# Kernel optimization log

Hardware: AMD Instinct MI355X
Metric: run time of the kernel (lower is better)

## Reference

```python
import jax, jax.numpy as jnp
import numpy as np

H = 2048       # hidden_size
NH = 16        # num_attention_heads
NKV = 4        # num_key_value_heads
HD = H // NH   # head_dim = 128
INTER = 8192   # intermediate_size
L = 2048       # packed sequence length
EPS = 1e-6


def rmsnorm(x, w, eps=EPS):
    var = jnp.mean(x * x, axis=-1, keepdims=True)
    return x * jax.lax.rsqrt(var + eps) * w


def setup_inputs() -> dict:
    key = jax.random.key(0)
    ks = jax.random.split(key, 9)
    s = 0.02
    return {
        "hidden_states": jax.random.normal(ks[0], (1, L, H), jnp.float32),
        "cu_seqlens_q": jnp.array([0, 512, 1280, 2048], jnp.int32),
        "ln1_w": jnp.ones((H,), jnp.float32),
        "ln2_w": jnp.ones((H,), jnp.float32),
        "q_w": jax.random.normal(ks[1], (NH * HD, H), jnp.float32) * s,
        "k_w": jax.random.normal(ks[2], (NKV * HD, H), jnp.float32) * s,
        "v_w": jax.random.normal(ks[3], (NKV * HD, H), jnp.float32) * s,
        "o_w": jax.random.normal(ks[4], (H, NH * HD), jnp.float32) * s,
        "gate_w": jax.random.normal(ks[5], (INTER, H), jnp.float32) * s,
        "up_w": jax.random.normal(ks[6], (INTER, H), jnp.float32) * s,
        "down_w": jax.random.normal(ks[7], (H, INTER), jnp.float32) * s,
    }


def _segment_mask(cu, q_len):
    # segment id of each position: repeat_interleave of arange over lengths
    pos = jnp.arange(q_len)
    seg = jnp.searchsorted(cu[1:], pos, side="right")  # [L]
    mask = seg[:, None] == seg[None, :]
    mask = mask & (pos[None, :] <= pos[:, None])  # causal, q_len == k_len
    return mask  # [L, L] bool


def _forward(hidden_states, cu_seqlens_q, ln1_w, ln2_w, q_w, k_w, v_w, o_w,
             gate_w, up_w, down_w):
    b, q_len, _ = hidden_states.shape
    residual = hidden_states
    normed = rmsnorm(hidden_states, ln1_w)

    # project_kv
    key_states = (normed @ k_w.T).reshape(b, q_len, NKV, HD)
    value_states = (normed @ v_w.T).reshape(b, q_len, NKV, HD)

    q = (normed @ q_w.T).reshape(b, q_len, NH, HD)
    rep = NH // NKV
    k = jnp.repeat(key_states, rep, axis=2)   # repeat_interleave over heads
    v = jnp.repeat(value_states, rep, axis=2)

    scores = jnp.einsum("bqhd,bkhd->bhqk", q, k) / np.sqrt(HD)
    mask = _segment_mask(cu_seqlens_q, q_len)
    scores = jnp.where(mask[None, None, :, :], scores,
                       jnp.finfo(scores.dtype).min)
    probs = jax.nn.softmax(scores.astype(jnp.float32), axis=-1).astype(q.dtype)
    attn = jnp.einsum("bhqk,bkhd->bqhd", probs, v).reshape(b, q_len, NH * HD)
    mixed = attn @ o_w.T

    hidden = residual + mixed
    residual = hidden
    normed2 = rmsnorm(hidden, ln2_w)
    mlp = (jax.nn.silu(normed2 @ gate_w.T) * (normed2 @ up_w.T)) @ down_w.T
    hidden = residual + mlp
    return hidden, key_states, value_states


def reference(hidden_states, cu_seqlens_q, ln1_w, ln2_w, q_w, k_w, v_w, o_w,
              gate_w, up_w, down_w):
    return _forward(hidden_states, cu_seqlens_q, ln1_w, ln2_w, q_w, k_w, v_w,
                    o_w, gate_w, up_w, down_w)
```

## Files before the change

kernel.cpp:

```cpp
#include <hip/hip_runtime.h>
#include <stdint.h>

typedef __bf16 bf16;
typedef __bf16 bf16x8 __attribute__((ext_vector_type(8)));
typedef __bf16 bf16x4v __attribute__((ext_vector_type(4)));
typedef float f32x4 __attribute__((ext_vector_type(4)));

#define L_SEQ 2048
#define H_DIM 2048
#define KV_DIM 512
#define QKV_LD 3072
#define INTER_DIM 8192

__device__ __forceinline__ void load_lds16(const void* g, void* l) {
  __builtin_amdgcn_global_load_lds(
      (const __attribute__((address_space(1))) void*)g,
      (__attribute__((address_space(3))) void*)l, 16, 0, 0);
}

__global__ __launch_bounds__(256)
void cvt_all(const float* __restrict__ q, const float* __restrict__ k,
             const float* __restrict__ v, const float* __restrict__ o,
             const float* __restrict__ g, const float* __restrict__ u,
             const float* __restrict__ dn, bf16* __restrict__ WB) {
// ... 96 lines not shown
                 const float* __restrict__ res, float* __restrict__ out) {
  const size_t i = ((size_t)blockIdx.x * 256 + threadIdx.x) * 4;
  float4 a = *(const float4*)(p + i);
  float4 b = *(const float4*)(p + zs + i);
  float4 c = *(const float4*)(p + 2 * zs + i);
  float4 d = *(const float4*)(p + 3 * zs + i);
  float4 r = *(const float4*)(res + i);
  float4 o;
  o.x = a.x + b.x + c.x + d.x + r.x;
  o.y = a.y + b.y + c.y + d.y + r.y;
  o.z = a.z + b.z + c.z + d.z + r.z;
  o.w = a.w + b.w + c.w + d.w + r.w;
  *(float4*)(out + i) = o;
}

__global__ __launch_bounds__(256)
void qkv_combine(const float* __restrict__ p, size_t zs,
                 bf16* __restrict__ qkv, float* __restrict__ outk,
                 float* __restrict__ outv) {
  const size_t i = ((size_t)blockIdx.x * 256 + threadIdx.x) * 4;
  float4 a = *(const float4*)(p + i);
  float4 b = *(const float4*)(p + zs + i);
  float4 s;
  s.x = a.x + b.x; s.y = a.y + b.y; s.z = a.z + b.z; s.w = a.w + b.w;
  bf16x4v o;
  o[0] = (bf16)s.x; o[1] = (bf16)s.y; o[2] = (bf16)s.z; o[3] = (bf16)s.w;
  *(bf16x4v*)(qkv + i) = o;
  const int col = (int)(i % QKV_LD);
  const size_t row = i / QKV_LD;
  if (col >= 2560)      *(float4*)(outv + row * KV_DIM + (col - 2560)) = s;
  else if (col >= 2048) *(float4*)(outk + row * KV_DIM + (col - 2048)) = s;
}

__global__ __launch_bounds__(256, 3)
void gemm_bt(const bf16* __restrict__ A, int lda,
             const bf16* __restrict__ B, int ldb, int kpb,
             float* __restrict__ outf, int ldof, size_t zstride) {
  __shared__ bf16 sA[2 * 128 * 32];
  __shared__ bf16 sB[2 * 128 * 32];
  const int t = threadIdx.x;
  const int lane = t & 63;
  const int l15 = lane & 15, l4 = lane >> 4;
  const int wm = ((t >> 6) >> 1) * 64;
  const int wn = ((t >> 6) & 1) * 64;
  const int m0 = blockIdx.y * 128;
  const int n0 = blockIdx.x * 128;
  const int kbeg = blockIdx.z * kpb;
  const int kend = kbeg + kpb;

  const f32x4 zero = {0.f, 0.f, 0.f, 0.f};
  f32x4 acc[4][4];
#pragma unroll
  for (int i = 0; i < 4; ++i)
#pragma unroll
    for (int j = 0; j < 4; ++j) acc[i][j] = zero;

  for (int k0 = kbeg; k0 < kend; k0 += 64) {
#pragma unroll
    for (int i = 0; i < 4; ++i) {
      const int flat = i * 4096 + t * 16;
      const int kc = flat >> 13;
      const int wb = flat & 8191;
      const int r = wb >> 6, ce = (wb & 63) >> 1;
      const int gc = k0 + kc * 32 + ce;
      load_lds16(A + (size_t)(m0 + r) * lda + gc, (char*)sA + flat);
      load_lds16(B + (size_t)(n0 + r) * ldb + gc, (char*)sB + flat);
// ... 6 lines not shown
#pragma unroll
      for (int mi = 0; mi < 4; ++mi)
        af[mi] = *(const bf16x8*)(&sA[kc * 4096 + (wm + mi * 16 + l15) * 32 +
                                      l4 * 8]);
#pragma unroll
      for (int ni = 0; ni < 4; ++ni)
        bfr[ni] = *(const bf16x8*)(&sB[kc * 4096 + (wn + ni * 16 + l15) * 32 +
                                       l4 * 8]);
#pragma unroll
      for (int mi = 0; mi < 4; ++mi)
#pragma unroll
        for (int ni = 0; ni < 4; ++ni)
          acc[mi][ni] = __builtin_amdgcn_mfma_f32_16x16x32_bf16(
              af[mi], bfr[ni], acc[mi][ni], 0, 0, 0);
    }
    __syncthreads();
  }

#pragma unroll
  for (int mi = 0; mi < 4; ++mi) {
#pragma unroll
    for (int ni = 0; ni < 4; ++ni) {
      const int row0 = m0 + wm + mi * 16 + l4 * 4;
      const int col = n0 + wn + ni * 16 + l15;
#pragma unroll
      for (int r = 0; r < 4; ++r)
        outf[zstride * blockIdx.z + (size_t)(row0 + r) * ldof + col] =
            acc[mi][ni][r];
    }
  }
}

__global__ __launch_bounds__(256, 2)
void gemm_glu(const bf16* __restrict__ A, const bf16* __restrict__ Bg,
              const bf16* __restrict__ Bu, bf16* __restrict__ out) {
  __shared__ bf16 sA[2 * 128 * 32];
  __shared__ bf16 sG[2 * 128 * 32];
  __shared__ bf16 sU[2 * 128 * 32];
  const int t = threadIdx.x;
  const int lane = t & 63;
  const int l15 = lane & 15, l4 = lane >> 4;
  const int wm = ((t >> 6) >> 1) * 64;
  const int wn = ((t >> 6) & 1) * 64;
  const int m0 = blockIdx.y * 128;
  const int n0 = blockIdx.x * 128;

  const f32x4 zero = {0.f, 0.f, 0.f, 0.f};
  f32x4 ag[4][4], au[4][4];
#pragma unroll
  for (int i = 0; i < 4; ++i)
#pragma unroll
    for (int j = 0; j < 4; ++j) { ag[i][j] = zero; au[i][j] = zero; }

  for (int k0 = 0; k0 < H_DIM; k0 += 64) {
#pragma unroll
    for (int i = 0; i < 4; ++i) {
      const int flat = i * 4096 + t * 16;
      const int kc = flat >> 13;
      const int wb = flat & 8191;
      const int r = wb >> 6, ce = (wb & 63) >> 1;
      const int gc = k0 + kc * 32 + ce;
      load_lds16(A + (size_t)(m0 + r) * H_DIM + gc, (char*)sA + flat);
      load_lds16(Bg + (size_t)(n0 + r) * H_DIM + gc, (char*)sG + flat);
      load_lds16(Bu + (size_t)(n0 + r) * H_DIM + gc, (char*)sU + flat);
    }
    __syncthreads();

#pragma unroll
    for (int kc = 0; kc < 2; ++kc) {
      bf16x8 af[4], bg[4], bu[4];
#pragma unroll
      for (int mi = 0; mi < 4; ++mi)
        af[mi] = *(const bf16x8*)(&sA[kc * 4096 + (wm + mi * 16 + l15) * 32 +
                                      l4 * 8]);
#pragma unroll
      for (int ni = 0; ni < 4; ++ni) {
        bg[ni] = *(const bf16x8*)(&sG[kc * 4096 + (wn + ni * 16 + l15) * 32 +
                                      l4 * 8]);
        bu[ni] = *(const bf16x8*)(&sU[kc * 4096 + (wn + ni * 16 + l15) * 32 +
                                      l4 * 8]);
      }
#pragma unroll
      for (int mi = 0; mi < 4; ++mi)
#pragma unroll
        for (int ni = 0; ni < 4; ++ni) {
          ag[mi][ni] = __builtin_amdgcn_mfma_f32_16x16x32_bf16(
              af[mi], bg[ni], ag[mi][ni], 0, 0, 0);
          au[mi][ni] = __builtin_amdgcn_mfma_f32_16x16x32_bf16(
              af[mi], bu[ni], au[mi][ni], 0, 0, 0);
        }
    }
    __syncthreads();
  }

#pragma unroll
  for (int mi = 0; mi < 4; ++mi) {
#pragma unroll
    for (int ni = 0; ni < 4; ++ni) {
      const int row0 = m0 + wm + mi * 16 + l4 * 4;
      const int col = n0 + wn + ni * 16 + l15;
#pragma unroll
      for (int r = 0; r < 4; ++r) {
        const float g = ag[mi][ni][r];
        const float u = au[mi][ni][r];
        const float s = g / (1.f + __expf(-g));
        out[(size_t)(row0 + r) * INTER_DIM + col] = (bf16)(s * u);
      }
    }
  }
}

__global__ __launch_bounds__(256, 2)
void attn_fwd(const bf16* __restrict__ qkv, const int* __restrict__ cu,
              bf16* __restrict__ out) {
  const int h = blockIdx.y;
  const int q0 = blockIdx.x * 64;
  const int kvh = h >> 2;
  const int t = threadIdx.x;
  const int lane = t & 63;
  const int w = t >> 6;
  const int l15 = lane & 15, l4 = lane >> 4;

  __shared__ bf16 sK[64 * 136];
  __shared__ bf16 sVt[128 * 72];
  __shared__ bf16 sP[4][16 * 64];

  const int c1 = cu[1], c2 = cu[2];
  const int seg0 = (q0 >= c2) ? c2 : ((q0 >= c1) ? c1 : 0);

  const int qrow = q0 + w * 16 + l15;
  bf16x8 qf[4];
#pragma unroll
  for (int kc = 0; kc < 4; ++kc) {
    bf16x8 v = *(const bf16x8*)(qkv + (size_t)qrow * QKV_LD + h * 128 +
                                kc * 32 + l4 * 8);
#pragma unroll
    for (int j = 0; j < 8; ++j)
      v[j] = (bf16)((float)v[j] * 0.08838834764831845f);
    qf[kc] = v;
  }

  const f32x4 zero = {0.f, 0.f, 0.f, 0.f};
  f32x4 oacc[8];
#pragma unroll
  for (int i = 0; i < 8; ++i) oacc[i] = zero;
// ... 123 lines not shown
  const float* o_w    = (const float*)d_in[7];
  const float* gate_w = (const float*)d_in[8];
  const float* up_w   = (const float*)d_in[9];
  const float* down_w = (const float*)d_in[10];

  float* out_hidden = (float*)d_out;
  float* out_k = out_hidden + (size_t)L_SEQ * H_DIM;
  float* out_v = out_k + (size_t)L_SEQ * KV_DIM;

  char* ws = (char*)d_ws;
  bf16* WB = (bf16*)ws;
  const size_t wq_off = 0;
  const size_t wo_off = 6291456;
  const size_t wg_off = 10485760;
  const size_t wu_off = 27262976;
  const size_t wd_off = 44040192;

  bf16*  normed1 = (bf16*)(ws + ((size_t)116 << 20));
  bf16*  qkv     = (bf16*)(ws + ((size_t)124 << 20));
  bf16*  attnb   = (bf16*)(ws + ((size_t)136 << 20));
  bf16*  normed2 = (bf16*)(ws + ((size_t)144 << 20));
  bf16*  interb  = (bf16*)(ws + ((size_t)152 << 20));
  float* qpart   = (float*)(ws + ((size_t)136 << 20));
  float* opart   = (float*)(ws + ((size_t)152 << 20));
  float* dpart   = (float*)(ws);

  dim3 blk(256);

  cvt_all<<<29696, blk, 0, stream>>>(q_w, k_w, v_w, o_w, gate_w, up_w, down_w,
                                     WB);

  rmsnorm_bf16<<<L_SEQ, blk, 0, stream>>>(hs, ln1, normed1);

  gemm_bt<<<dim3(24, 16, 2), blk, 0, stream>>>(
      normed1, H_DIM, WB + wq_off, H_DIM, 1024, qpart, QKV_LD,
      (size_t)L_SEQ * QKV_LD);
  qkv_combine<<<6144, blk, 0, stream>>>(qpart, (size_t)L_SEQ * QKV_LD, qkv,
                                        out_k, out_v);

  attn_fwd<<<dim3(32, 16), blk, 0, stream>>>(qkv, cu, attnb);

  gemm_bt<<<dim3(16, 16, 2), blk, 0, stream>>>(
      attnb, H_DIM, WB + wo_off, H_DIM, 1024, opart, H_DIM,
      (size_t)L_SEQ * H_DIM);

  add_rmsnorm<<<L_SEQ, blk, 0, stream>>>(opart, opart + (size_t)L_SEQ * H_DIM,
                                         hs, ln2, out_hidden, normed2);

  gemm_glu<<<dim3(64, 16), blk, 0, stream>>>(normed2, WB + wg_off, WB + wu_off,
                                             interb);

  gemm_bt<<<dim3(16, 16, 4), blk, 0, stream>>>(
      interb, INTER_DIM, WB + wd_off, INTER_DIM, 2048, dpart, H_DIM,
      (size_t)L_SEQ * H_DIM);

  reduce_add4<<<4096, blk, 0, stream>>>(dpart, (size_t)L_SEQ * H_DIM,
                                        out_hidden, out_hidden);
}
```

Measured before the change: 653.0 us.

## Use 256x256-tile 8-wave GEMMs with triple-buffered LDS pipeline

Replaces the 128x128 four-wave GEMM kernels for the QKV, GLU and down projections with 512-thread kernels using 256-row tiles. These kernels keep a triple-buffered LDS ring filled by async global-to-LDS loads, use XOR-swizzled LDS layouts, and split each K-step into two MFMA phases with raised priority and explicit barriers. A block-ID swizzle is added for L2 locality. The GLU variant stages the up results through LDS so gate and up are combined after the loop. The aim is more reuse per byte loaded and better overlap of loads with MFMA work, at the cost of fewer workgroups and more register and LDS pressure.

```diff
diff --git a/kernel.cpp b/kernel.cpp
--- a/kernel.cpp
+++ b/kernel.cpp
@@ -152,6 +152,260 @@
   else if (col >= 2048) *(float4*)(outk + row * KV_DIM + (col - 2048)) = s;
 }
 
+
+__device__ __forceinline__ void stage_round(const bf16* __restrict__ P,
+                                            int ld, int grow0, int k0,
+                                            char* ldsdst, int t) {
+  const int flat = t * 16;
+  const int row = flat >> 6;
+  const int w = flat & 63;
+  const int kk = (w ^ ((row & 3) << 4)) >> 1;
+  load_lds16(P + (size_t)(grow0 + row) * ld + k0 + kk, ldsdst + flat);
+}
+
+__device__ __forceinline__ bf16x8 frag_ld(const bf16* __restrict__ sl,
+                                          int row, int l4) {
+  return *(const bf16x8*)(sl + row * 32 + ((l4 ^ (row & 3)) << 3));
+}
+
+#define PHASE_SYNC_PRE()                                  \
+  __builtin_amdgcn_sched_barrier(0);                      \
+  __builtin_amdgcn_s_barrier();                           \
+  asm volatile("s_waitcnt lgkmcnt(0)" ::: "memory");      \
+  __builtin_amdgcn_sched_barrier(0);                      \
+  __builtin_amdgcn_s_setprio(1)
+
+#define PHASE_SYNC_POST()                                 \
+  __builtin_amdgcn_s_setprio(0);                          \
+  __builtin_amdgcn_sched_barrier(0)
+
+__global__ __launch_bounds__(512, 2)
+void gemm8_bt(const bf16* __restrict__ A, int lda,
+              const bf16* __restrict__ B, int ldb, int kpb,
+              float* __restrict__ outf, int ldof, size_t zstride) {
+  __shared__ __align__(16) char smem[98304];
+  bf16* sA = (bf16*)smem;
+  bf16* sB = (bf16*)(smem + 49152);
+  const int t = threadIdx.x;
+  const int lane = t & 63;
+  const int l15 = lane & 15, l4 = lane >> 4;
+  const int wid = t >> 6;
+  const int wr = wid >> 2, wc = wid & 3;
+
+  const int nwg = gridDim.x * gridDim.y;
+  const int bid = blockIdx.y * gridDim.x + blockIdx.x;
+  const int swz = (bid & 7) * (nwg >> 3) + (bid >> 3);
+  const int m0 = (swz / gridDim.x) * 256;
+  const int n0 = (swz % gridDim.x) * 256;
+  const int kbeg = blockIdx.z * kpb;
+  const int NT = kpb >> 5;
+
+  const f32x4 zero = {0.f, 0.f, 0.f, 0.f};
+  f32x4 acc[8][4];
+#pragma unroll
+  for (int m = 0; m < 8; ++m)
+#pragma unroll
+    for (int n = 0; n < 4; ++n) acc[m][n] = zero;
+
+  stage_round(A, lda, m0, kbeg, (char*)sA, t);
+  stage_round(A, lda, m0 + 128, kbeg, (char*)sA + 8192, t);
+  stage_round(B, ldb, n0, kbeg, (char*)sB, t);
+  stage_round(B, ldb, n0 + 128, kbeg, (char*)sB + 8192, t);
+  stage_round(A, lda, m0, kbeg + 32, (char*)sA + 16384, t);
+  stage_round(A, lda, m0 + 128, kbeg + 32, (char*)sA + 16384 + 8192, t);
+  stage_round(B, ldb, n0, kbeg + 32, (char*)sB + 16384, t);
+  stage_round(B, ldb, n0 + 128, kbeg + 32, (char*)sB + 16384 + 8192, t);
+  asm volatile("s_waitcnt vmcnt(4)" ::: "memory");
+  __builtin_amdgcn_s_barrier();
+
+  int cur = 0, s2 = 2;
+  for (int tt = 0; tt < NT; ++tt) {
+    const bf16* sAc = sA + cur * 8192;
+    const bf16* sBc = sB + cur * 8192;
+    const int k2 = kbeg + (tt + 2) * 32;
+    bf16x8 af[4], bfr[4];
+#pragma unroll
+    for (int n = 0; n < 4; ++n)
+      bfr[n] = frag_ld(sBc, wc * 64 + n * 16 + l15, l4);
+#pragma unroll
+    for (int m = 0; m < 4; ++m)
+      af[m] = frag_ld(sAc, wr * 128 + m * 16 + l15, l4);
+    if (tt + 2 < NT) {
+      char* d = (char*)(sA + s2 * 8192);
+      stage_round(A, lda, m0, k2, d, t);
+      stage_round(A, lda, m0 + 128, k2, d + 8192, t);
+    }
+    PHASE_SYNC_PRE();
+#pragma unroll
+    for (int m = 0; m < 4; ++m)
+#pragma unroll
+      for (int n = 0; n < 4; ++n)
+        acc[m][n] = __builtin_amdgcn_mfma_f32_16x16x32_bf16(
+            af[m], bfr[n], acc[m][n], 0, 0, 0);
+    PHASE_SYNC_POST();
+    __builtin_amdgcn_s_barrier();
+#pragma unroll
+    for (int m = 0; m < 4; ++m)
+      af[m] = frag_ld(sAc, wr * 128 + 64 + m * 16 + l15, l4);
+    if (tt + 2 < NT) {
+      char* d = (char*)(sB + s2 * 8192);
+      stage_round(B, ldb, n0, k2, d, t);
+      stage_round(B, ldb, n0 + 128, k2, d + 8192, t);
+    }
+    PHASE_SYNC_PRE();
+#pragma unroll
+    for (int m = 0; m < 4; ++m)
+#pragma unroll
+      for (int n = 0; n < 4; ++n)
+        acc[4 + m][n] = __builtin_amdgcn_mfma_f32_16x16x32_bf16(
+            af[m], bfr[n], acc[4 + m][n], 0, 0, 0);
+    PHASE_SYNC_POST();
+    if (tt + 2 < NT)
+      asm volatile("s_waitcnt vmcnt(4)" ::: "memory");
+    else if (tt + 1 < NT)
+      asm volatile("s_waitcnt vmcnt(0)" ::: "memory");
+    __builtin_amdgcn_s_barrier();
+    cur = (cur == 2) ? 0 : cur + 1;
+    s2 = (s2 == 2) ? 0 : s2 + 1;
+  }
+
+  float* outz = outf + zstride * blockIdx.z;
+#pragma unroll
+  for (int m = 0; m < 8; ++m)
+#pragma unroll
+    for (int n = 0; n < 4; ++n) {
+      const int row0 = m0 + wr * 128 + m * 16 + l4 * 4;
+      const int col = n0 + wc * 64 + n * 16 + l15;
+#pragma unroll
+      for (int r = 0; r < 4; ++r)
+        outz[(size_t)(row0 + r) * ldof + col] = acc[m][n][r];
+    }
+}
+
+__global__ __launch_bounds__(512, 2)
+void gemm8_glu(const bf16* __restrict__ A, const bf16* __restrict__ Bg,
+               const bf16* __restrict__ Bu, bf16* __restrict__ out) {
+  __shared__ __align__(16) char smem[98304];
+  bf16* sA = (bf16*)smem;
+  bf16* sB = (bf16*)(smem + 49152);
+  const int t = threadIdx.x;
+  const int lane = t & 63;
+  const int l15 = lane & 15, l4 = lane >> 4;
+  const int wid = t >> 6;
+  const int wr = wid >> 2, wc = wid & 3;
+
+  const int nwg = gridDim.x * gridDim.y;
+  const int bid = blockIdx.y * gridDim.x + blockIdx.x;
+  const int swz = (bid & 7) * (nwg >> 3) + (bid >> 3);
+  const int m0 = (swz / gridDim.x) * 256;
+  const int n0 = (swz % gridDim.x) * 128;
+
+  const f32x4 zero = {0.f, 0.f, 0.f, 0.f};
+  f32x4 acc[8][4];
+#pragma unroll
+  for (int m = 0; m < 8; ++m)
+#pragma unroll
+    for (int n = 0; n < 4; ++n) acc[m][n] = zero;
+
+  stage_round(A, H_DIM, m0, 0, (char*)sA, t);
+  stage_round(A, H_DIM, m0 + 128, 0, (char*)sA + 8192, t);
+  stage_round(Bg, H_DIM, n0, 0, (char*)sB, t);
+  stage_round(Bu, H_DIM, n0, 0, (char*)sB + 8192, t);
+  stage_round(A, H_DIM, m0, 32, (char*)sA + 16384, t);
+  stage_round(A, H_DIM, m0 + 128, 32, (char*)sA + 16384 + 8192, t);
+  stage_round(Bg, H_DIM, n0, 32, (char*)sB + 16384, t);
+  stage_round(Bu, H_DIM, n0, 32, (char*)sB + 16384 + 8192, t);
+  asm volatile("s_waitcnt vmcnt(4)" ::: "memory");
+  __builtin_amdgcn_s_barrier();
+
+  int cur = 0, s2 = 2;
+  const int NT = H_DIM / 32;
+  for (int tt = 0; tt < NT; ++tt) {
+    const bf16* sAc = sA + cur * 8192;
+    const bf16* sBc = sB + cur * 8192;
+    const int k2 = (tt + 2) * 32;
+    bf16x8 af[4], bfr[4];
+#pragma unroll
+    for (int n = 0; n < 4; ++n)
+      bfr[n] = frag_ld(sBc, wc * 64 + n * 16 + l15, l4);
+#pragma unroll
+    for (int m = 0; m < 4; ++m)
+      af[m] = frag_ld(sAc, wr * 128 + m * 16 + l15, l4);
+    if (tt + 2 < NT) {
+      char* d = (char*)(sA + s2 * 8192);
+      stage_round(A, H_DIM, m0, k2, d, t);
+      stage_round(A, H_DIM, m0 + 128, k2, d + 8192, t);
+    }
+    PHASE_SYNC_PRE();
+#pragma unroll
+    for (int m = 0; m < 4; ++m)
+#pragma unroll
+      for (int n = 0; n < 4; ++n)
+        acc[m][n] = __builtin_amdgcn_mfma_f32_16x16x32_bf16(
+            af[m], bfr[n], acc[m][n], 0, 0, 0);
+    PHASE_SYNC_POST();
+    __builtin_amdgcn_s_barrier();
+#pragma unroll
+    for (int m = 0; m < 4; ++m)
+      af[m] = frag_ld(sAc, wr * 128 + 64 + m * 16 + l15, l4);
+    if (tt + 2 < NT) {
+      char* d = (char*)(sB + s2 * 8192);
+      stage_round(Bg, H_DIM, n0, k2, d, t);
+      stage_round(Bu, H_DIM, n0, k2, d + 8192, t);
+    }
+    PHASE_SYNC_PRE();
+#pragma unroll
+    for (int m = 0; m < 4; ++m)
+#pragma unroll
+      for (int n = 0; n < 4; ++n)
+        acc[4 + m][n] = __builtin_amdgcn_mfma_f32_16x16x32_bf16(
+            af[m], bfr[n], acc[4 + m][n], 0, 0, 0);
+    PHASE_SYNC_POST();
+    if (tt + 2 < NT)
+      asm volatile("s_waitcnt vmcnt(4)" ::: "memory");
+    else if (tt + 1 < NT)
+      asm volatile("s_waitcnt vmcnt(0)" ::: "memory");
+    __builtin_amdgcn_s_barrier();
+    cur = (cur == 2) ? 0 : cur + 1;
+    s2 = (s2 == 2) ? 0 : s2 + 1;
+  }
+
+  float* upf = (float*)smem;
+  const int isUp = (wc >= 2);
+  const int colL = (isUp ? (wc - 2) : wc) * 64;
+#pragma unroll
+  for (int c = 0; c < 2; ++c) {
+    __syncthreads();
+    if (isUp) {
+#pragma unroll
+      for (int m = 0; m < 4; ++m)
+#pragma unroll
+        for (int n = 0; n < 4; ++n)
+#pragma unroll
+          for (int r = 0; r < 4; ++r)
+            upf[(wr * 64 + m * 16 + l4 * 4 + r) * 129 + colL + n * 16 + l15] =
+                acc[c * 4 + m][n][r];
+    }
+    __syncthreads();
+    if (!isUp) {
+#pragma unroll
+      for (int m = 0; m < 4; ++m)
+#pragma unroll
+        for (int n = 0; n < 4; ++n)
+#pragma unroll
+          for (int r = 0; r < 4; ++r) {
+            const float g = acc[c * 4 + m][n][r];
+            const float u = upf[(wr * 64 + m * 16 + l4 * 4 + r) * 129 + colL +
+                                n * 16 + l15];
+            const float sg = g / (1.f + __expf(-g));
+            out[(size_t)(m0 + wr * 128 + c * 64 + m * 16 + l4 * 4 + r) *
+                    INTER_DIM +
+                n0 + colL + n * 16 + l15] = (bf16)(sg * u);
+          }
+    }
+  }
+}
+
 __global__ __launch_bounds__(256, 3)
 void gemm_bt(const bf16* __restrict__ A, int lda,
              const bf16* __restrict__ B, int ldb, int kpb,
@@ -224,85 +478,6 @@
 }
 
 __global__ __launch_bounds__(256, 2)
-void gemm_glu(const bf16* __restrict__ A, const bf16* __restrict__ Bg,
-              const bf16* __restrict__ Bu, bf16* __restrict__ out) {
-  __shared__ bf16 sA[2 * 128 * 32];
-  __shared__ bf16 sG[2 * 128 * 32];
-  __shared__ bf16 sU[2 * 128 * 32];
-  const int t = threadIdx.x;
-  const int lane = t & 63;
-  const int l15 = lane & 15, l4 = lane >> 4;
-  const int wm = ((t >> 6) >> 1) * 64;
-  const int wn = ((t >> 6) & 1) * 64;
-  const int m0 = blockIdx.y * 128;
-  const int n0 = blockIdx.x * 128;
-
-  const f32x4 zero = {0.f, 0.f, 0.f, 0.f};
-  f32x4 ag[4][4], au[4][4];
-#pragma unroll
-  for (int i = 0; i < 4; ++i)
-#pragma unroll
-    for (int j = 0; j < 4; ++j) { ag[i][j] = zero; au[i][j] = zero; }
-
-  for (int k0 = 0; k0 < H_DIM; k0 += 64) {
-#pragma unroll
-    for (int i = 0; i < 4; ++i) {
-      const int flat = i * 4096 + t * 16;
-      const int kc = flat >> 13;
-      const int wb = flat & 8191;
-      const int r = wb >> 6, ce = (wb & 63) >> 1;
-      const int gc = k0 + kc * 32 + ce;
-      load_lds16(A + (size_t)(m0 + r) * H_DIM + gc, (char*)sA + flat);
-      load_lds16(Bg + (size_t)(n0 + r) * H_DIM + gc, (char*)sG + flat);
-      load_lds16(Bu + (size_t)(n0 + r) * H_DIM + gc, (char*)sU + flat);
-    }
-    __syncthreads();
-
-#pragma unroll
-    for (int kc = 0; kc < 2; ++kc) {
-      bf16x8 af[4], bg[4], bu[4];
-#pragma unroll
-      for (int mi = 0; mi < 4; ++mi)
-        af[mi] = *(const bf16x8*)(&sA[kc * 4096 + (wm + mi * 16 + l15) * 32 +
-                                      l4 * 8]);
-#pragma unroll
-      for (int ni = 0; ni < 4; ++ni) {
-        bg[ni] = *(const bf16x8*)(&sG[kc * 4096 + (wn + ni * 16 + l15) * 32 +
-                                      l4 * 8]);
-        bu[ni] = *(const bf16x8*)(&sU[kc * 4096 + (wn + ni * 16 + l15) * 32 +
-                                      l4 * 8]);
-      }
-#pragma unroll
-      for (int mi = 0; mi < 4; ++mi)
-#pragma unroll
-        for (int ni = 0; ni < 4; ++ni) {
-          ag[mi][ni] = __builtin_amdgcn_mfma_f32_16x16x32_bf16(
-              af[mi], bg[ni], ag[mi][ni], 0, 0, 0);
-          au[mi][ni] = __builtin_amdgcn_mfma_f32_16x16x32_bf16(
-              af[mi], bu[ni], au[mi][ni], 0, 0, 0);
-        }
-    }
-    __syncthreads();
-  }
-
-#pragma unroll
-  for (int mi = 0; mi < 4; ++mi) {
-#pragma unroll
-    for (int ni = 0; ni < 4; ++ni) {
-      const int row0 = m0 + wm + mi * 16 + l4 * 4;
-      const int col = n0 + wn + ni * 16 + l15;
-#pragma unroll
-      for (int r = 0; r < 4; ++r) {
-        const float g = ag[mi][ni][r];
-        const float u = au[mi][ni][r];
-        const float s = g / (1.f + __expf(-g));
-        out[(size_t)(row0 + r) * INTER_DIM + col] = (bf16)(s * u);
-      }
-    }
-  }
-}
-
-__global__ __launch_bounds__(256, 2)
 void attn_fwd(const bf16* __restrict__ qkv, const int* __restrict__ cu,
               bf16* __restrict__ out) {
   const int h = blockIdx.y;
@@ -492,7 +667,7 @@
 
   rmsnorm_bf16<<<L_SEQ, blk, 0, stream>>>(hs, ln1, normed1);
 
-  gemm_bt<<<dim3(24, 16, 2), blk, 0, stream>>>(
+  gemm8_bt<<<dim3(12, 8, 2), dim3(512), 0, stream>>>(
       normed1, H_DIM, WB + wq_off, H_DIM, 1024, qpart, QKV_LD,
       (size_t)L_SEQ * QKV_LD);
   qkv_combine<<<6144, blk, 0, stream>>>(qpart, (size_t)L_SEQ * QKV_LD, qkv,
@@ -507,10 +682,10 @@
   add_rmsnorm<<<L_SEQ, blk, 0, stream>>>(opart, opart + (size_t)L_SEQ * H_DIM,
                                          hs, ln2, out_hidden, normed2);
 
-  gemm_glu<<<dim3(64, 16), blk, 0, stream>>>(normed2, WB + wg_off, WB + wu_off,
-                                             interb);
-
-  gemm_bt<<<dim3(16, 16, 4), blk, 0, stream>>>(
+  gemm8_glu<<<dim3(64, 8), dim3(512), 0, stream>>>(normed2, WB + wg_off,
+                                                   WB + wu_off, interb);
+
+  gemm8_bt<<<dim3(8, 8, 4), dim3(512), 0, stream>>>(
       interb, INTER_DIM, WB + wd_off, INTER_DIM, 2048, dpart, H_DIM,
       (size_t)L_SEQ * H_DIM);
 
```

Result: faster. 624.2 us (-4.4%).

## Add 256x256-tile 8-wave GEMM kernels with swizzled LDS and pipelined loads

Applied to the files above, without the earlier changes.

Introduces gemm8_bt and gemm8_glu: 512-thread blocks computing 256x256 (or 256x128 gate/up) tiles, XOR-swizzled LDS layout, double-buffered direct-to-LDS loads interleaved with four MFMA quadrants, s_setprio and explicit waitcnts, plus block-index remapping for L2 locality. These replace the 128x128 kernels for the QKV, gate/up and down projections, raising arithmetic intensity and overlapping global loads with compute. The larger tiles use 128KB of LDS and many registers, which limits occupancy and yields fewer blocks (e.g. 192 for QKV), which may underfill the CUs.

```diff
diff --git a/kernel.cpp b/kernel.cpp
--- a/kernel.cpp
+++ b/kernel.cpp
@@ -152,6 +152,325 @@
   else if (col >= 2048) *(float4*)(outk + row * KV_DIM + (col - 2048)) = s;
 }
 
+
+#define LOAD_A(halfp)                                                      \
+  _Pragma("unroll") for (int mi = 0; mi < 4; ++mi)                         \
+      _Pragma("unroll") for (int kc = 0; kc < 2; ++kc)                     \
+          af[mi][kc] = *(const bf16x8*)((halfp) + aoff[mi][kc]);
+
+#define LOAD_B(nh, halfp)                                                  \
+  _Pragma("unroll") for (int ni = 0; ni < 2; ++ni)                         \
+      _Pragma("unroll") for (int kc = 0; kc < 2; ++kc)                     \
+          bfv[nh][ni][kc] = *(const bf16x8*)((halfp) + boff[ni][kc]);
+
+#define MFMA_QUAD(mh, nh)                                                  \
+  _Pragma("unroll") for (int mi = 0; mi < 4; ++mi)                         \
+      _Pragma("unroll") for (int ni = 0; ni < 2; ++ni)                     \
+          _Pragma("unroll") for (int kc = 0; kc < 2; ++kc)                 \
+              acc[mh][nh][mi][ni] = __builtin_amdgcn_mfma_f32_16x16x32_bf16( \
+                  af[mi][kc], bfv[nh][ni][kc], acc[mh][nh][mi][ni], 0, 0, 0);
+
+#define WAIT_LGKM0()                                      \
+  asm volatile("s_waitcnt lgkmcnt(0)" ::: "memory");      \
+  __builtin_amdgcn_sched_barrier(0)
+
+#define WAIT_VM(n)                                        \
+  asm volatile("s_waitcnt vmcnt(" #n ")" ::: "memory");   \
+  __builtin_amdgcn_sched_barrier(0)
+
+__global__ __launch_bounds__(512, 2)
+void gemm8_bt(const bf16* __restrict__ A, int lda,
+              const bf16* __restrict__ B, int ldb, int kpb,
+              float* __restrict__ outf, int ldof, size_t zstride) {
+  __shared__ __align__(16) bf16 smem[65536];
+  bf16* sA = smem;
+  bf16* sB = smem + 32768;
+  char* smb = (char*)smem;
+  const int t = threadIdx.x;
+  const int lane = t & 63;
+  const int l15 = lane & 15, l4 = lane >> 4;
+  const int wid = t >> 6;
+  const int wr = wid >> 2, wc = wid & 3;
+
+  const int gn = gridDim.x, gm = gridDim.y;
+  const int bid = blockIdx.y * gn + blockIdx.x;
+  int mb, nb;
+  if ((gn & 7) == 0) {
+    const int j = bid & 7, local = bid >> 3, npx = gn >> 3;
+    nb = j * npx + local % npx;
+    mb = local / npx;
+  } else {
+    nb = bid % gn;
+    mb = bid / gn;
+  }
+  const int m0 = mb * 256, n0 = nb * 256;
+  const int kbeg = blockIdx.z * kpb;
+  const int NT = kpb >> 6;
+
+  int aoff[4][2], boff[2][2];
+#pragma unroll
+  for (int mi = 0; mi < 4; ++mi)
+#pragma unroll
+    for (int kc = 0; kc < 2; ++kc)
+      aoff[mi][kc] = (wr * 64 + mi * 16 + l15) * 64 +
+                     ((((kc << 2) | l4) ^ (l15 & 7)) << 3);
+#pragma unroll
+  for (int ni = 0; ni < 2; ++ni)
+#pragma unroll
+    for (int kc = 0; kc < 2; ++kc)
+      boff[ni][kc] = (wc * 32 + ni * 16 + l15) * 64 +
+                     ((((kc << 2) | l4) ^ (l15 & 7)) << 3);
+
+  const int rr = t >> 3;
+  const int gs8 = (((t & 7) ^ (rr & 7)) << 3);
+  const bf16* pa = A + (size_t)(m0 + rr) * lda + gs8;
+  const bf16* pb = B + (size_t)(n0 + rr) * ldb + gs8;
+  const size_t la = (size_t)64 * lda, lb = (size_t)64 * ldb;
+  const int dln = t * 16;
+
+  {
+    const size_t ko = (size_t)kbeg;
+    load_lds16(pa + ko,          smb + dln);
+    load_lds16(pa + ko + la,     smb + 8192 + dln);
+    load_lds16(pb + ko,          smb + 65536 + dln);
+    load_lds16(pb + ko + lb,     smb + 65536 + 8192 + dln);
+    load_lds16(pb + ko + 2 * lb, smb + 65536 + 16384 + dln);
+    load_lds16(pb + ko + 3 * lb, smb + 65536 + 16384 + 8192 + dln);
+    load_lds16(pa + ko + 2 * la, smb + 16384 + dln);
+    load_lds16(pa + ko + 3 * la, smb + 16384 + 8192 + dln);
+  }
+
+  const f32x4 zero = {0.f, 0.f, 0.f, 0.f};
+  f32x4 acc[2][2][4][2];
+#pragma unroll
+  for (int mh = 0; mh < 2; ++mh)
+#pragma unroll
+    for (int nh = 0; nh < 2; ++nh)
+#pragma unroll
+      for (int mi = 0; mi < 4; ++mi)
+#pragma unroll
+        for (int ni = 0; ni < 2; ++ni) acc[mh][nh][mi][ni] = zero;
+
+  bf16x8 af[4][2], bfv[2][2][2];
+
+  for (int tt = 0; tt < NT; ++tt) {
+    const int cur = tt & 1, nxt = cur ^ 1;
+    const bf16* A0p = sA + cur * 16384;
+    const bf16* A1p = A0p + 8192;
+    const bf16* B0p = sB + cur * 16384;
+    const bf16* B1p = B0p + 8192;
+    char* dA = smb + nxt * 32768;
+    char* dB = smb + 65536 + nxt * 32768;
+    const size_t ko = (size_t)kbeg + (size_t)(tt + 1) * 64;
+    const bool st = (tt + 1 < NT);
+
+    WAIT_VM(4);
+    __builtin_amdgcn_s_barrier();
+    LOAD_A(A0p);
+    LOAD_B(0, B0p);
+    if (st) {
+      load_lds16(pa + ko,      dA + dln);
+      load_lds16(pa + ko + la, dA + 8192 + dln);
+    }
+    WAIT_LGKM0();
+    __builtin_amdgcn_s_setprio(1);
+    MFMA_QUAD(0, 0);
+    __builtin_amdgcn_s_setprio(0);
+
+    if (st) { WAIT_VM(4); } else { WAIT_VM(2); }
+    __builtin_amdgcn_s_barrier();
+    LOAD_B(1, B1p);
+    if (st) {
+      load_lds16(pb + ko,      dB + dln);
+      load_lds16(pb + ko + lb, dB + 8192 + dln);
+    }
+    WAIT_LGKM0();
+    __builtin_amdgcn_s_setprio(1);
+    MFMA_QUAD(0, 1);
+    __builtin_amdgcn_s_setprio(0);
+
+    if (st) { WAIT_VM(4); } else { WAIT_VM(0); }
+    __builtin_amdgcn_s_barrier();
+    LOAD_A(A1p);
+    if (st) {
+      load_lds16(pb + ko + 2 * lb, dB + 16384 + dln);
+      load_lds16(pb + ko + 3 * lb, dB + 16384 + 8192 + dln);
+    }
+    WAIT_LGKM0();
+    __builtin_amdgcn_s_setprio(1);
+    MFMA_QUAD(1, 0);
+    __builtin_amdgcn_s_setprio(0);
+
+    __builtin_amdgcn_s_barrier();
+    if (st) {
+      load_lds16(pa + ko + 2 * la, dA + 16384 + dln);
+      load_lds16(pa + ko + 3 * la, dA + 16384 + 8192 + dln);
+    }
+    __builtin_amdgcn_s_setprio(1);
+    MFMA_QUAD(1, 1);
+    __builtin_amdgcn_s_setprio(0);
+    __builtin_amdgcn_sched_barrier(0);
+  }
+
+  float* outz = outf + zstride * blockIdx.z;
+#pragma unroll
+  for (int mh = 0; mh < 2; ++mh)
+#pragma unroll
+    for (int nh = 0; nh < 2; ++nh)
+#pragma unroll
+      for (int mi = 0; mi < 4; ++mi)
+#pragma unroll
+        for (int ni = 0; ni < 2; ++ni) {
+          const int row0 = m0 + mh * 128 + wr * 64 + mi * 16 + l4 * 4;
+          const int col = n0 + nh * 128 + wc * 32 + ni * 16 + l15;
+#pragma unroll
+          for (int r = 0; r < 4; ++r)
+            outz[(size_t)(row0 + r) * ldof + col] = acc[mh][nh][mi][ni][r];
+        }
+}
+
+__global__ __launch_bounds__(512, 2)
+void gemm8_glu(const bf16* __restrict__ A, const bf16* __restrict__ Bg,
+               const bf16* __restrict__ Bu, bf16* __restrict__ out) {
+  __shared__ __align__(16) bf16 smem[65536];
+  bf16* sA = smem;
+  bf16* sB = smem + 32768;
+  char* smb = (char*)smem;
+  const int t = threadIdx.x;
+  const int lane = t & 63;
+  const int l15 = lane & 15, l4 = lane >> 4;
+  const int wid = t >> 6;
+  const int wr = wid >> 2, wc = wid & 3;
+
+  const int gn = gridDim.x;
+  const int bid = blockIdx.y * gn + blockIdx.x;
+  const int j = bid & 7, local = bid >> 3, npx = gn >> 3;
+  const int nb = j * npx + local % npx;
+  const int mb = local / npx;
+  const int m0 = mb * 256, n0 = nb * 128;
+  const int NT = H_DIM / 64;
+
+  int aoff[4][2], boff[2][2];
+#pragma unroll
+  for (int mi = 0; mi < 4; ++mi)
+#pragma unroll
+    for (int kc = 0; kc < 2; ++kc)
+      aoff[mi][kc] = (wr * 64 + mi * 16 + l15) * 64 +
+                     ((((kc << 2) | l4) ^ (l15 & 7)) << 3);
+#pragma unroll
+  for (int ni = 0; ni < 2; ++ni)
+#pragma unroll
+    for (int kc = 0; kc < 2; ++kc)
+      boff[ni][kc] = (wc * 32 + ni * 16 + l15) * 64 +
+                     ((((kc << 2) | l4) ^ (l15 & 7)) << 3);
+
+  const int rr = t >> 3;
+  const int gs8 = (((t & 7) ^ (rr & 7)) << 3);
+  const bf16* pa = A + (size_t)(m0 + rr) * H_DIM + gs8;
+  const bf16* pg = Bg + (size_t)(n0 + rr) * H_DIM + gs8;
+  const bf16* pu = Bu + (size_t)(n0 + rr) * H_DIM + gs8;
+  const size_t la = (size_t)64 * H_DIM;
+  const int dln = t * 16;
+
+  load_lds16(pa,          smb + dln);
+  load_lds16(pa + la,     smb + 8192 + dln);
+  load_lds16(pg,          smb + 65536 + dln);
+  load_lds16(pg + la,     smb + 65536 + 8192 + dln);
+  load_lds16(pu,          smb + 65536 + 16384 + dln);
+  load_lds16(pu + la,     smb + 65536 + 16384 + 8192 + dln);
+  load_lds16(pa + 2 * la, smb + 16384 + dln);
+  load_lds16(pa + 3 * la, smb + 16384 + 8192 + dln);
+
+  const f32x4 zero = {0.f, 0.f, 0.f, 0.f};
+  f32x4 acc[2][2][4][2];
+#pragma unroll
+  for (int mh = 0; mh < 2; ++mh)
+#pragma unroll
+    for (int nh = 0; nh < 2; ++nh)
+#pragma unroll
+      for (int mi = 0; mi < 4; ++mi)
+#pragma unroll
+        for (int ni = 0; ni < 2; ++ni) acc[mh][nh][mi][ni] = zero;
+
+  bf16x8 af[4][2], bfv[2][2][2];
+
+  for (int tt = 0; tt < NT; ++tt) {
+    const int cur = tt & 1, nxt = cur ^ 1;
+    const bf16* A0p = sA + cur * 16384;
+    const bf16* A1p = A0p + 8192;
+    const bf16* B0p = sB + cur * 16384;
+    const bf16* B1p = B0p + 8192;
+    char* dA = smb + nxt * 32768;
+    char* dB = smb + 65536 + nxt * 32768;
+    const size_t ko = (size_t)(tt + 1) * 64;
+    const bool st = (tt + 1 < NT);
+
+    WAIT_VM(4);
+    __builtin_amdgcn_s_barrier();
+    LOAD_A(A0p);
+    LOAD_B(0, B0p);
+    if (st) {
+      load_lds16(pa + ko,      dA + dln);
+      load_lds16(pa + ko + la, dA + 8192 + dln);
+    }
+    WAIT_LGKM0();
+    __builtin_amdgcn_s_setprio(1);
+    MFMA_QUAD(0, 0);
+    __builtin_amdgcn_s_setprio(0);
+
+    if (st) { WAIT_VM(4); } else { WAIT_VM(2); }
+    __builtin_amdgcn_s_barrier();
+    LOAD_B(1, B1p);
+    if (st) {
+      load_lds16(pg + ko,      dB + dln);
+      load_lds16(pg + ko + la, dB + 8192 + dln);
+    }
+    WAIT_LGKM0();
+    __builtin_amdgcn_s_setprio(1);
+    MFMA_QUAD(0, 1);
+    __builtin_amdgcn_s_setprio(0);
+
+    if (st) { WAIT_VM(4); } else { WAIT_VM(0); }
+    __builtin_amdgcn_s_barrier();
+    LOAD_A(A1p);
+    if (st) {
+      load_lds16(pu + ko,      dB + 16384 + dln);
+      load_lds16(pu + ko + la, dB + 16384 + 8192 + dln);
+    }
+    WAIT_LGKM0();
+    __builtin_amdgcn_s_setprio(1);
+    MFMA_QUAD(1, 0);
+    __builtin_amdgcn_s_setprio(0);
+
+    __builtin_amdgcn_s_barrier();
+    if (st) {
+      load_lds16(pa + ko + 2 * la, dA + 16384 + dln);
+      load_lds16(pa + ko + 3 * la, dA + 16384 + 8192 + dln);
+    }
+    __builtin_amdgcn_s_setprio(1);
+    MFMA_QUAD(1, 1);
+    __builtin_amdgcn_s_setprio(0);
+    __builtin_amdgcn_sched_barrier(0);
+  }
+
+#pragma unroll
+  for (int mh = 0; mh < 2; ++mh)
+#pragma unroll
+    for (int mi = 0; mi < 4; ++mi)
+#pragma unroll
+      for (int ni = 0; ni < 2; ++ni) {
+        const int row0 = m0 + mh * 128 + wr * 64 + mi * 16 + l4 * 4;
+        const int col = n0 + wc * 32 + ni * 16 + l15;
+#pragma unroll
+        for (int r = 0; r < 4; ++r) {
+          const float g = acc[mh][0][mi][ni][r];
+          const float u = acc[mh][1][mi][ni][r];
+          const float sg = g / (1.f + __expf(-g));
+          out[(size_t)(row0 + r) * INTER_DIM + col] = (bf16)(sg * u);
+        }
+      }
+}
+
 __global__ __launch_bounds__(256, 3)
 void gemm_bt(const bf16* __restrict__ A, int lda,
              const bf16* __restrict__ B, int ldb, int kpb,
@@ -224,85 +543,6 @@
 }
 
 __global__ __launch_bounds__(256, 2)
-void gemm_glu(const bf16* __restrict__ A, const bf16* __restrict__ Bg,
-              const bf16* __restrict__ Bu, bf16* __restrict__ out) {
-  __shared__ bf16 sA[2 * 128 * 32];
-  __shared__ bf16 sG[2 * 128 * 32];
-  __shared__ bf16 sU[2 * 128 * 32];
-  const int t = threadIdx.x;
-  const int lane = t & 63;
-  const int l15 = lane & 15, l4 = lane >> 4;
-  const int wm = ((t >> 6) >> 1) * 64;
-  const int wn = ((t >> 6) & 1) * 64;
-  const int m0 = blockIdx.y * 128;
-  const int n0 = blockIdx.x * 128;
-
-  const f32x4 zero = {0.f, 0.f, 0.f, 0.f};
-  f32x4 ag[4][4], au[4][4];
-#pragma unroll
-  for (int i = 0; i < 4; ++i)
-#pragma unroll
-    for (int j = 0; j < 4; ++j) { ag[i][j] = zero; au[i][j] = zero; }
-
-  for (int k0 = 0; k0 < H_DIM; k0 += 64) {
-#pragma unroll
-    for (int i = 0; i < 4; ++i) {
-      const int flat = i * 4096 + t * 16;
-      const int kc = flat >> 13;
-      const int wb = flat & 8191;
-      const int r = wb >> 6, ce = (wb & 63) >> 1;
-      const int gc = k0 + kc * 32 + ce;
-      load_lds16(A + (size_t)(m0 + r) * H_DIM + gc, (char*)sA + flat);
-      load_lds16(Bg + (size_t)(n0 + r) * H_DIM + gc, (char*)sG + flat);
-      load_lds16(Bu + (size_t)(n0 + r) * H_DIM + gc, (char*)sU + flat);
-    }
-    __syncthreads();
-
-#pragma unroll
-    for (int kc = 0; kc < 2; ++kc) {
-      bf16x8 af[4], bg[4], bu[4];
-#pragma unroll
-      for (int mi = 0; mi < 4; ++mi)
-        af[mi] = *(const bf16x8*)(&sA[kc * 4096 + (wm + mi * 16 + l15) * 32 +
-                                      l4 * 8]);
-#pragma unroll
-      for (int ni = 0; ni < 4; ++ni) {
-        bg[ni] = *(const bf16x8*)(&sG[kc * 4096 + (wn + ni * 16 + l15) * 32 +
-                                      l4 * 8]);
-        bu[ni] = *(const bf16x8*)(&sU[kc * 4096 + (wn + ni * 16 + l15) * 32 +
-                                      l4 * 8]);
-      }
-#pragma unroll
-      for (int mi = 0; mi < 4; ++mi)
-#pragma unroll
-        for (int ni = 0; ni < 4; ++ni) {
-          ag[mi][ni] = __builtin_amdgcn_mfma_f32_16x16x32_bf16(
-              af[mi], bg[ni], ag[mi][ni], 0, 0, 0);
-          au[mi][ni] = __builtin_amdgcn_mfma_f32_16x16x32_bf16(
-              af[mi], bu[ni], au[mi][ni], 0, 0, 0);
-        }
-    }
-    __syncthreads();
-  }
-
-#pragma unroll
-  for (int mi = 0; mi < 4; ++mi) {
-#pragma unroll
-    for (int ni = 0; ni < 4; ++ni) {
-      const int row0 = m0 + wm + mi * 16 + l4 * 4;
-      const int col = n0 + wn + ni * 16 + l15;
-#pragma unroll
-      for (int r = 0; r < 4; ++r) {
-        const float g = ag[mi][ni][r];
-        const float u = au[mi][ni][r];
-        const float s = g / (1.f + __expf(-g));
-        out[(size_t)(row0 + r) * INTER_DIM + col] = (bf16)(s * u);
-      }
-    }
-  }
-}
-
-__global__ __launch_bounds__(256, 2)
 void attn_fwd(const bf16* __restrict__ qkv, const int* __restrict__ cu,
               bf16* __restrict__ out) {
   const int h = blockIdx.y;
@@ -492,7 +732,7 @@
 
   rmsnorm_bf16<<<L_SEQ, blk, 0, stream>>>(hs, ln1, normed1);
 
-  gemm_bt<<<dim3(24, 16, 2), blk, 0, stream>>>(
+  gemm8_bt<<<dim3(12, 8, 2), dim3(512), 0, stream>>>(
       normed1, H_DIM, WB + wq_off, H_DIM, 1024, qpart, QKV_LD,
       (size_t)L_SEQ * QKV_LD);
   qkv_combine<<<6144, blk, 0, stream>>>(qpart, (size_t)L_SEQ * QKV_LD, qkv,
@@ -507,10 +747,10 @@
   add_rmsnorm<<<L_SEQ, blk, 0, stream>>>(opart, opart + (size_t)L_SEQ * H_DIM,
                                          hs, ln2, out_hidden, normed2);
 
-  gemm_glu<<<dim3(64, 16), blk, 0, stream>>>(normed2, WB + wg_off, WB + wu_off,
-                                             interb);
-
-  gemm_bt<<<dim3(16, 16, 4), blk, 0, stream>>>(
+  gemm8_glu<<<dim3(64, 8), dim3(512), 0, stream>>>(normed2, WB + wg_off,
+                                                   WB + wu_off, interb);
+
+  gemm8_bt<<<dim3(8, 8, 4), dim3(512), 0, stream>>>(
       interb, INTER_DIM, WB + wd_off, INTER_DIM, 2048, dpart, H_DIM,
       (size_t)L_SEQ * H_DIM);
 
```

After: 576.5 us. -11.7%, faster.

## Add 256x256-tile 512-thread GEMMs with triple-buffered async LDS loads

Applied to the files above, without the earlier changes.

Introduces new GEMM kernels using 512-thread blocks with 256x256 output tiles (256x128 for the fused gate/up GLU), a three-stage LDS ring of global_load_lds prefetches synchronized by vmcnt waits plus a single barrier per k-step, XOR-swizzled LDS layout to avoid bank conflicts, and grouped block-index remapping for L2 reuse. They replace the QKV, GLU and down-projection GEMMs; the O-projection still uses the old kernel. The aim is higher arithmetic intensity per LDS byte and hidden load latency, at the cost of 96KB of LDS per block, more registers, and fewer blocks in flight.

```diff
diff --git a/kernel.cpp b/kernel.cpp
--- a/kernel.cpp
+++ b/kernel.cpp
@@ -152,6 +152,240 @@
   else if (col >= 2048) *(float4*)(outk + row * KV_DIM + (col - 2048)) = s;
 }
 
+
+#define WAIT_VM(n) asm volatile("s_waitcnt vmcnt(" #n ")" ::: "memory")
+
+#define ISSUE_TILE(ko, base)                          \
+  load_lds16(pa0 + (ko), (base) + dln);               \
+  load_lds16(pa1 + (ko), (base) + 8192 + dln);        \
+  load_lds16(pb0 + (ko), (base) + 16384 + dln);       \
+  load_lds16(pb1 + (ko), (base) + 24576 + dln);
+
+#define MFMA_Q(mh, nh, bfr)                                                  \
+  _Pragma("unroll") for (int mi = 0; mi < 4; ++mi)                           \
+      _Pragma("unroll") for (int ni = 0; ni < 2; ++ni)                       \
+          acc[mh][nh][mi][ni] = __builtin_amdgcn_mfma_f32_16x16x32_bf16(     \
+              af[mi], bfr[ni], acc[mh][nh][mi][ni], 0, 0, 0);
+
+__global__ __launch_bounds__(512, 2)
+void gemm32_bt(const bf16* __restrict__ A, int lda,
+               const bf16* __restrict__ B, int ldb, int kpb,
+               float* __restrict__ outf, int ldof, size_t zstride) {
+  __shared__ __align__(16) char smb[98304];
+  const int t = threadIdx.x;
+  const int lane = t & 63;
+  const int l15 = lane & 15, l4 = lane >> 4;
+  const int wid = t >> 6;
+  const int wr = wid >> 2, wc = wid & 3;
+
+  const int gn = gridDim.x;
+  const int bid = blockIdx.y * gn + blockIdx.x;
+  int mb, nb;
+  if ((gn & 7) == 0) {
+    const int j = bid & 7, local = bid >> 3, npx = gn >> 3;
+    nb = j * npx + local % npx;
+    mb = local / npx;
+  } else {
+    nb = bid % gn;
+    mb = bid / gn;
+  }
+  const int m0 = mb * 256, n0 = nb * 256;
+  const int kbeg = blockIdx.z * kpb;
+  const int NT = kpb >> 5;
+
+  int aoff[4], boff[2];
+#pragma unroll
+  for (int mi = 0; mi < 4; ++mi) {
+    const int rA = wr * 64 + mi * 16 + l15;
+    aoff[mi] = rA * 64 + ((l4 ^ ((rA >> 1) & 3)) << 4);
+  }
+#pragma unroll
+  for (int ni = 0; ni < 2; ++ni) {
+    const int rB = wc * 32 + ni * 16 + l15;
+    boff[ni] = rB * 64 + ((l4 ^ ((rB >> 1) & 3)) << 4);
+  }
+
+  const int r = t >> 2;
+  const int gsw = (((t & 3) ^ ((r >> 1) & 3)) << 3);
+  const bf16* pa0 = A + (size_t)(m0 + r) * lda + kbeg + gsw;
+  const bf16* pa1 = A + (size_t)(m0 + 128 + r) * lda + kbeg + gsw;
+  const bf16* pb0 = B + (size_t)(n0 + r) * ldb + kbeg + gsw;
+  const bf16* pb1 = B + (size_t)(n0 + 128 + r) * ldb + kbeg + gsw;
+  const int dln = t * 16;
+
+  ISSUE_TILE(0, smb);
+  if (NT > 1) { ISSUE_TILE(32, smb + 32768); }
+
+  const f32x4 zero = {0.f, 0.f, 0.f, 0.f};
+  f32x4 acc[2][2][4][2];
+#pragma unroll
+  for (int mh = 0; mh < 2; ++mh)
+#pragma unroll
+    for (int nh = 0; nh < 2; ++nh)
+#pragma unroll
+      for (int mi = 0; mi < 4; ++mi)
+#pragma unroll
+        for (int ni = 0; ni < 2; ++ni) acc[mh][nh][mi][ni] = zero;
+
+  int br = 0, bw = 2;
+#pragma unroll 1
+  for (int tt = 0; tt < NT; ++tt) {
+    if (tt + 1 < NT) { WAIT_VM(4); } else { WAIT_VM(0); }
+    __builtin_amdgcn_s_barrier();
+    if (tt + 2 < NT) {
+      char* dst = smb + bw * 32768;
+      const int ko = (tt + 2) * 32;
+      ISSUE_TILE(ko, dst);
+    }
+    const char* bb = smb + br * 32768;
+    const char* cA0 = bb;
+    const char* cA1 = bb + 8192;
+    const char* cB0 = bb + 16384;
+    const char* cB1 = bb + 24576;
+
+    bf16x8 af[4], b0f[2], b1f[2];
+#pragma unroll
+    for (int mi = 0; mi < 4; ++mi)
+      af[mi] = *(const bf16x8*)(cA0 + aoff[mi]);
+#pragma unroll
+    for (int ni = 0; ni < 2; ++ni) b0f[ni] = *(const bf16x8*)(cB0 + boff[ni]);
+#pragma unroll
+    for (int ni = 0; ni < 2; ++ni) b1f[ni] = *(const bf16x8*)(cB1 + boff[ni]);
+    MFMA_Q(0, 0, b0f);
+    MFMA_Q(0, 1, b1f);
+#pragma unroll
+    for (int mi = 0; mi < 4; ++mi)
+      af[mi] = *(const bf16x8*)(cA1 + aoff[mi]);
+    MFMA_Q(1, 0, b0f);
+    MFMA_Q(1, 1, b1f);
+
+    br = (br == 2) ? 0 : br + 1;
+    bw = (bw == 2) ? 0 : bw + 1;
+  }
+
+  float* outz = outf + zstride * blockIdx.z;
+#pragma unroll
+  for (int mh = 0; mh < 2; ++mh)
+#pragma unroll
+    for (int nh = 0; nh < 2; ++nh)
+#pragma unroll
+      for (int mi = 0; mi < 4; ++mi)
+#pragma unroll
+        for (int ni = 0; ni < 2; ++ni) {
+          const int row0 = m0 + mh * 128 + wr * 64 + mi * 16 + l4 * 4;
+          const int col = n0 + nh * 128 + wc * 32 + ni * 16 + l15;
+#pragma unroll
+          for (int rr2 = 0; rr2 < 4; ++rr2)
+            outz[(size_t)(row0 + rr2) * ldof + col] = acc[mh][nh][mi][ni][rr2];
+        }
+}
+
+__global__ __launch_bounds__(512, 2)
+void gemm32_glu(const bf16* __restrict__ A, const bf16* __restrict__ Bg,
+                const bf16* __restrict__ Bu, bf16* __restrict__ out) {
+  __shared__ __align__(16) char smb[98304];
+  const int t = threadIdx.x;
+  const int lane = t & 63;
+  const int l15 = lane & 15, l4 = lane >> 4;
+  const int wid = t >> 6;
+  const int wr = wid >> 2, wc = wid & 3;
+
+  const int gn = gridDim.x;
+  const int bid = blockIdx.y * gn + blockIdx.x;
+  const int j = bid & 7, local = bid >> 3, npx = gn >> 3;
+  const int nb = j * npx + local % npx;
+  const int mb = local / npx;
+  const int m0 = mb * 256, n0 = nb * 128;
+  const int NT = H_DIM / 32;
+
+  int aoff[4], boff[2];
+#pragma unroll
+  for (int mi = 0; mi < 4; ++mi) {
+    const int rA = wr * 64 + mi * 16 + l15;
+    aoff[mi] = rA * 64 + ((l4 ^ ((rA >> 1) & 3)) << 4);
+  }
+#pragma unroll
+  for (int ni = 0; ni < 2; ++ni) {
+    const int rB = wc * 32 + ni * 16 + l15;
+    boff[ni] = rB * 64 + ((l4 ^ ((rB >> 1) & 3)) << 4);
+  }
+
+  const int r = t >> 2;
+  const int gsw = (((t & 3) ^ ((r >> 1) & 3)) << 3);
+  const bf16* pa0 = A + (size_t)(m0 + r) * H_DIM + gsw;
+  const bf16* pa1 = A + (size_t)(m0 + 128 + r) * H_DIM + gsw;
+  const bf16* pb0 = Bg + (size_t)(n0 + r) * H_DIM + gsw;
+  const bf16* pb1 = Bu + (size_t)(n0 + r) * H_DIM + gsw;
+  const int dln = t * 16;
+
+  ISSUE_TILE(0, smb);
+  ISSUE_TILE(32, smb + 32768);
+
+  const f32x4 zero = {0.f, 0.f, 0.f, 0.f};
+  f32x4 acc[2][2][4][2];
+#pragma unroll
+  for (int mh = 0; mh < 2; ++mh)
+#pragma unroll
+    for (int nh = 0; nh < 2; ++nh)
+#pragma unroll
+      for (int mi = 0; mi < 4; ++mi)
+#pragma unroll
+        for (int ni = 0; ni < 2; ++ni) acc[mh][nh][mi][ni] = zero;
+
+  int br = 0, bw = 2;
+#pragma unroll 1
+  for (int tt = 0; tt < NT; ++tt) {
+    if (tt + 1 < NT) { WAIT_VM(4); } else { WAIT_VM(0); }
+    __builtin_amdgcn_s_barrier();
+    if (tt + 2 < NT) {
+      char* dst = smb + bw * 32768;
+      const int ko = (tt + 2) * 32;
+      ISSUE_TILE(ko, dst);
+    }
+    const char* bb = smb + br * 32768;
+    const char* cA0 = bb;
+    const char* cA1 = bb + 8192;
+    const char* cB0 = bb + 16384;
+    const char* cB1 = bb + 24576;
+
+    bf16x8 af[4], b0f[2], b1f[2];
+#pragma unroll
+    for (int mi = 0; mi < 4; ++mi)
+      af[mi] = *(const bf16x8*)(cA0 + aoff[mi]);
+#pragma unroll
+    for (int ni = 0; ni < 2; ++ni) b0f[ni] = *(const bf16x8*)(cB0 + boff[ni]);
+#pragma unroll
+    for (int ni = 0; ni < 2; ++ni) b1f[ni] = *(const bf16x8*)(cB1 + boff[ni]);
+    MFMA_Q(0, 0, b0f);
+    MFMA_Q(0, 1, b1f);
+#pragma unroll
+    for (int mi = 0; mi < 4; ++mi)
+      af[mi] = *(const bf16x8*)(cA1 + aoff[mi]);
+    MFMA_Q(1, 0, b0f);
+    MFMA_Q(1, 1, b1f);
+
+    br = (br == 2) ? 0 : br + 1;
+    bw = (bw == 2) ? 0 : bw + 1;
+  }
+
+#pragma unroll
+  for (int mh = 0; mh < 2; ++mh)
+#pragma unroll
+    for (int mi = 0; mi < 4; ++mi)
+#pragma unroll
+      for (int ni = 0; ni < 2; ++ni) {
+        const int row0 = m0 + mh * 128 + wr * 64 + mi * 16 + l4 * 4;
+        const int col = n0 + wc * 32 + ni * 16 + l15;
+#pragma unroll
+        for (int rr2 = 0; rr2 < 4; ++rr2) {
+          const float g = acc[mh][0][mi][ni][rr2];
+          const float u = acc[mh][1][mi][ni][rr2];
+          const float sg = g / (1.f + __expf(-g));
+          out[(size_t)(row0 + rr2) * INTER_DIM + col] = (bf16)(sg * u);
+        }
+      }
+}
+
 __global__ __launch_bounds__(256, 3)
 void gemm_bt(const bf16* __restrict__ A, int lda,
              const bf16* __restrict__ B, int ldb, int kpb,
@@ -224,85 +458,6 @@
 }
 
 __global__ __launch_bounds__(256, 2)
-void gemm_glu(const bf16* __restrict__ A, const bf16* __restrict__ Bg,
-              const bf16* __restrict__ Bu, bf16* __restrict__ out) {
-  __shared__ bf16 sA[2 * 128 * 32];
-  __shared__ bf16 sG[2 * 128 * 32];
-  __shared__ bf16 sU[2 * 128 * 32];
-  const int t = threadIdx.x;
-  const int lane = t & 63;
-  const int l15 = lane & 15, l4 = lane >> 4;
-  const int wm = ((t >> 6) >> 1) * 64;
-  const int wn = ((t >> 6) & 1) * 64;
-  const int m0 = blockIdx.y * 128;
-  const int n0 = blockIdx.x * 128;
-
-  const f32x4 zero = {0.f, 0.f, 0.f, 0.f};
-  f32x4 ag[4][4], au[4][4];
-#pragma unroll
-  for (int i = 0; i < 4; ++i)
-#pragma unroll
-    for (int j = 0; j < 4; ++j) { ag[i][j] = zero; au[i][j] = zero; }
-
-  for (int k0 = 0; k0 < H_DIM; k0 += 64) {
-#pragma unroll
-    for (int i = 0; i < 4; ++i) {
-      const int flat = i * 4096 + t * 16;
-      const int kc = flat >> 13;
-      const int wb = flat & 8191;
-      const int r = wb >> 6, ce = (wb & 63) >> 1;
-      const int gc = k0 + kc * 32 + ce;
-      load_lds16(A + (size_t)(m0 + r) * H_DIM + gc, (char*)sA + flat);
-      load_lds16(Bg + (size_t)(n0 + r) * H_DIM + gc, (char*)sG + flat);
-      load_lds16(Bu + (size_t)(n0 + r) * H_DIM + gc, (char*)sU + flat);
-    }
-    __syncthreads();
-
-#pragma unroll
-    for (int kc = 0; kc < 2; ++kc) {
-      bf16x8 af[4], bg[4], bu[4];
-#pragma unroll
-      for (int mi = 0; mi < 4; ++mi)
-        af[mi] = *(const bf16x8*)(&sA[kc * 4096 + (wm + mi * 16 + l15) * 32 +
-                                      l4 * 8]);
-#pragma unroll
-      for (int ni = 0; ni < 4; ++ni) {
-        bg[ni] = *(const bf16x8*)(&sG[kc * 4096 + (wn + ni * 16 + l15) * 32 +
-                                      l4 * 8]);
-        bu[ni] = *(const bf16x8*)(&sU[kc * 4096 + (wn + ni * 16 + l15) * 32 +
-                                      l4 * 8]);
-      }
-#pragma unroll
-      for (int mi = 0; mi < 4; ++mi)
-#pragma unroll
-        for (int ni = 0; ni < 4; ++ni) {
-          ag[mi][ni] = __builtin_amdgcn_mfma_f32_16x16x32_bf16(
-              af[mi], bg[ni], ag[mi][ni], 0, 0, 0);
-          au[mi][ni] = __builtin_amdgcn_mfma_f32_16x16x32_bf16(
-              af[mi], bu[ni], au[mi][ni], 0, 0, 0);
-        }
-    }
-    __syncthreads();
-  }
-
-#pragma unroll
-  for (int mi = 0; mi < 4; ++mi) {
-#pragma unroll
-    for (int ni = 0; ni < 4; ++ni) {
-      const int row0 = m0 + wm + mi * 16 + l4 * 4;
-      const int col = n0 + wn + ni * 16 + l15;
-#pragma unroll
-      for (int r = 0; r < 4; ++r) {
-        const float g = ag[mi][ni][r];
-        const float u = au[mi][ni][r];
-        const float s = g / (1.f + __expf(-g));
-        out[(size_t)(row0 + r) * INTER_DIM + col] = (bf16)(s * u);
-      }
-    }
-  }
-}
-
-__global__ __launch_bounds__(256, 2)
 void attn_fwd(const bf16* __restrict__ qkv, const int* __restrict__ cu,
               bf16* __restrict__ out) {
   const int h = blockIdx.y;
@@ -492,7 +647,7 @@
 
   rmsnorm_bf16<<<L_SEQ, blk, 0, stream>>>(hs, ln1, normed1);
 
-  gemm_bt<<<dim3(24, 16, 2), blk, 0, stream>>>(
+  gemm32_bt<<<dim3(12, 8, 2), dim3(512), 0, stream>>>(
       normed1, H_DIM, WB + wq_off, H_DIM, 1024, qpart, QKV_LD,
       (size_t)L_SEQ * QKV_LD);
   qkv_combine<<<6144, blk, 0, stream>>>(qpart, (size_t)L_SEQ * QKV_LD, qkv,
@@ -507,10 +662,10 @@
   add_rmsnorm<<<L_SEQ, blk, 0, stream>>>(opart, opart + (size_t)L_SEQ * H_DIM,
                                          hs, ln2, out_hidden, normed2);
 
-  gemm_glu<<<dim3(64, 16), blk, 0, stream>>>(normed2, WB + wg_off, WB + wu_off,
-                                             interb);
-
-  gemm_bt<<<dim3(16, 16, 4), blk, 0, stream>>>(
+  gemm32_glu<<<dim3(64, 8), dim3(512), 0, stream>>>(normed2, WB + wg_off,
+                                                    WB + wu_off, interb);
+
+  gemm32_bt<<<dim3(8, 8, 4), dim3(512), 0, stream>>>(
       interb, INTER_DIM, WB + wd_off, INTER_DIM, 2048, dpart, H_DIM,
       (size_t)L_SEQ * H_DIM);
 
```

Result: faster. 594.6 us (-8.9%).
